# Performance work log

Measured on AMD Instinct MI355X. Metric: run time of the kernel, lower is better.

## Reference

```python
import jax, jax.numpy as jnp
import numpy as np

B, K, D = 8192, 8192, 512

def setup_inputs() -> dict:
    key = jax.random.key(0)
    k1, k2 = jax.random.split(key)
    z_e = jax.random.normal(k1, (B, D), dtype=jnp.float32)
    # codebook: kaiming-uniform-initialized parameter; random normal scaled similarly is fine for a numeric baseline
    codebook = jax.random.normal(k2, (K, D), dtype=jnp.float32)
    return {"z_e": z_e, "codebook": codebook}

def reference(z_e, codebook):
    # Euclidean distances via dot-product expansion (same math as
    # torch.norm(z_e[:,None]-codebook[None], dim=-1) without the [B,K,D] intermediate):
    # d^2 = ||z||^2 - 2 z.c + ||c||^2
    z_sq = jnp.sum(z_e * z_e, axis=-1, keepdims=True)          # [B,1]
    c_sq = jnp.sum(codebook * codebook, axis=-1)               # [K]
    cross = jnp.einsum('bd,kd->bk', z_e, codebook)             # [B,K] GEMM
    d2 = jnp.maximum(z_sq - 2.0 * cross + c_sq[None, :], 0.0)  # clamp fp negatives
    distances = jnp.sqrt(d2)                                   # [B,K]
    indices = jnp.argmin(distances, axis=-1)                   # [B]
    z_q = jnp.take(codebook, indices, axis=0)                  # [B,D] gather
    return (z_q, indices)
```

## Files before the change

### kernel.cpp

```cpp
#include <hip/hip_runtime.h>


constexpr int Bn = 8192;
constexpr int Kn = 8192;
constexpr int Dn = 512;

using half8  = __attribute__((ext_vector_type(8)))  _Float16;
using f32x16 = __attribute__((ext_vector_type(16))) float;

#define WS_CSQ  0u
#define WS_ZSQ  (32u*1024u)
#define WS_MAX  (64u*1024u)
#define WS_CNT  (64u*1024u + 64u)
#define WS_WL   (96u*1024u)
#define WS_PART (1u*1024u*1024u)
#define WS_P2   WS_PART
#define WS_CIMG (10u*1024u*1024u)
#define WS_ZIMG (18u*1024u*1024u)
#define WS_CEXT (26u*1024u*1024u)

typedef __attribute__((address_space(3))) void       as3_void;
typedef const __attribute__((address_space(1))) void as1_cvoid;

#define MFMA16 __builtin_amdgcn_mfma_f32_32x32x16_f16


__global__ __launch_bounds__(256) void prep_sums(const float* __restrict__ Z,
                                                 const float* __restrict__ Cb,
                                                 char* __restrict__ ws) {
  const int w = threadIdx.x >> 6, lane = threadIdx.x & 63;
  const int rid = blockIdx.x * 4 + w;
  if (blockIdx.x == 0 && threadIdx.x == 0) *(int*)(ws + WS_CNT) = 0;
  const bool isZ = rid < Bn;
  const int r = isZ ? rid : rid - Bn;
  const float* src = (isZ ? Z : Cb) + (size_t)r * Dn + lane * 8;
  const float4 v0 = *reinterpret_cast<const float4*>(src);
  const float4 v1 = *reinterpret_cast<const float4*>(src + 4);
  float ss = v0.x * v0.x + v0.y * v0.y + v0.z * v0.z + v0.w * v0.w +
             v1.x * v1.x + v1.y * v1.y + v1.z * v1.z + v1.w * v1.w;
#pragma unroll
  for (int off = 32; off; off >>= 1) ss += __shfl_xor(ss, off);
  if (lane == 0) {
    if (isZ) ((float*)(ws + WS_ZSQ))[r] = ss;
    else {
      ((float*)(ws + WS_CSQ))[r] = ss;
      atomicMax((int*)(ws + WS_MAX), __float_as_int(ss));
    }
  }
}

__global__ __launch_bounds__(256) void prep_img(const float* __restrict__ Z,
                                                const float* __restrict__ Cb,
                                                char* __restrict__ ws) {
  const int w = threadIdx.x >> 6, lane = threadIdx.x & 63;
  const int wid = blockIdx.x * 4 + w;
  char* CI = ws + WS_CIMG;
  char* ZI = ws + WS_ZIMG;
  char* CE = ws + WS_CEXT;
  if (wid < 2048) {
    const bool isC = wid < 1024;
    const int f = isC ? wid : wid - 1024;
    const int koct = f & 3;
    const int grp = isC ? ((f >> 2) & 3) : ((f >> 2) & 7);
    const int blk = isC ? (f >> 4) : (f >> 5);
    const int rowbase = (isC ? blk * 128 : blk * 256) + grp * 32;
    const float* src = isC ? Cb : Z;
    char* img = isC ? CI : ZI;
    const int fr = isC ? 256 : 512;
    const int ktsel = lane & 1, rr = lane >> 1;
    const float* rowp = src + (size_t)(rowbase + rr) * Dn;
#pragma unroll
    for (int kp = 0; kp < 4; ++kp) {
      const int kt = koct * 8 + kp * 2 + ktsel;
      const float4 v0 = *reinterpret_cast<const float4*>(rowp + kt * 16);
      const float4 v1 = *reinterpret_cast<const float4*>(rowp + kt * 16 + 4);
      const float4 v2 = *reinterpret_cast<const float4*>(rowp + kt * 16 + 8);
      const float4 v3 = *reinterpret_cast<const float4*>(rowp + kt * 16 + 12);
      const float fl[16] = {v0.x, v0.y, v0.z, v0.w, v1.x, v1.y, v1.z, v1.w,
                            v2.x, v2.y, v2.z, v2.w, v3.x, v3.y, v3.z, v3.w};
      _Float16 h[16];
#pragma unroll
      for (int j = 0; j < 16; ++j) h[j] = (_Float16)fl[j];
      const half8 lo8 = {h[0], h[1], h[2], h[3], h[4], h[5], h[6], h[7]};
      const half8 hi8 = {h[8], h[9], h[10], h[11], h[12], h[13], h[14], h[15]};
      char* fb = img + ((size_t)(blk * 32 + kt) * fr + grp * 64) * 16;
      *reinterpret_cast<half8*>(fb + rr * 16) = lo8;
      *reinterpret_cast<half8*>(fb + 512 + rr * 16) = hi8;
    }
  } else {
    const int e = wid - 2048;
    const int grp = e & 3, blk = e >> 2;
    half8 ev = {};
    if (lane < 32) {
      const float ss = ((const float*)(ws + WS_CSQ))[blk * 128 + grp * 32 + lane];
      const _Float16 hi = (_Float16)(-0.5f * ss);
      ev[0] = hi;
      ev[1] = (_Float16)(-0.5f * ss - (float)hi);
    }
    char* fb = CE + (size_t)(blk * 4 + grp) * 1024;
    *reinterpret_cast<half8*>(fb + lane * 16) = ev;
  }
}

__global__ __launch_bounds__(256, 2) void vq_pass1(char* __restrict__ ws) {
  __shared__ uint4 lds4[4096];
  char* lds = (char*)lds4;
  const int t = threadIdx.x, lane = t & 63, w = t >> 6;
  const int wm = w >> 1, wn = w & 1;
  const int bid = blockIdx.x;
  const int zblk = (bid & 7) * 4 + ((bid >> 3) & 3);
  const int split = bid >> 5;
  const int r31 = lane & 31, kh = lane >> 5;
  const size_t l16 = (size_t)lane * 16;

  const char* zsrcT = ws + WS_ZIMG + (size_t)zblk * 262144 + (size_t)w * 2048 + l16;
  char* const ldsW = lds + w * 2048;
  const char* APt = ws + WS_CIMG + (size_t)(split * 4) * 131072 + wm * 2048 + l16;
  const char* EbT = ws + WS_CEXT + (size_t)(split * 4) * 4096 + wm * 2048 + l16;
  const char* ldsRd = lds + wn * 4096 + kh * 512 + r31 * 16;

  half8 aset[4][2], aE[2];
  half8 bext = {};
  if (kh == 0) { bext[0] = (_Float16)1.f; bext[1] = (_Float16)1.f; }

  float qm1[4], qm2[4];
  int qi[4];
#pragma unroll
  for (int nb = 0; nb < 4; ++nb) { qm1[nb] = -3e38f; qm2[nb] = -3e38f; qi[nb] = 0x7fffffff; }
  f32x16 acc[2][4] = {};

#define GLDS(S, D) __builtin_amdgcn_global_load_lds((as1_cvoid*)(S), (as3_void*)(D), 16, 0, 0)

  GLDS(zsrcT, ldsW); GLDS(zsrcT + 1024, ldsW + 1024);
  aset[0][0] = *reinterpret_cast<const half8*>(APt);
  aset[0][1] = *reinterpret_cast<const half8*>(APt + 1024);
  GLDS(zsrcT + 8192, ldsW + 16384); GLDS(zsrcT + 8192 + 1024, ldsW + 16384 + 1024);
  aset[1][0] = *reinterpret_cast<const half8*>(APt + 4096);
  aset[1][1] = *reinterpret_cast<const half8*>(APt + 4096 + 1024);
  aE[0] = *reinterpret_cast<const half8*>(EbT);
  aE[1] = *reinterpret_cast<const half8*>(EbT + 1024);
  asm volatile("s_waitcnt vmcnt(8)" ::: "memory");
  __builtin_amdgcn_s_barrier();

  for (int p = 0; p < 4; ++p) {
#pragma unroll
    for (int kt = 0; kt < 32; ++kt) {
      {
        const char* An = (kt < 30) ? APt + (kt + 2) * 4096
                                   : APt + 131072 + (kt - 30) * 4096;
        aset[(kt + 2) & 3][0] = *reinterpret_cast<const half8*>(An);
        aset[(kt + 2) & 3][1] = *reinterpret_cast<const half8*>(An + 1024);
      }
      {
        const char* zs = zsrcT + ((kt + 2) & 31) * 8192;
        char* zd = ldsW + ((kt + 2) & 3) * 16384;
        GLDS(zs, zd); GLDS(zs + 1024, zd + 1024);
      }
      {
        const char* bb = ldsRd + (kt & 3) * 16384;
        const half8 b0 = *reinterpret_cast<const half8*>(bb);
        const half8 b1 = *reinterpret_cast<const half8*>(bb + 1024);
        const half8 b2 = *reinterpret_cast<const half8*>(bb + 2048);
        const half8 b3 = *reinterpret_cast<const half8*>(bb + 3072);
        const half8 a0 = aset[kt & 3][0];
        const half8 a1 = aset[kt & 3][1];
        acc[0][0] = MFMA16(a0, b0, acc[0][0], 0, 0, 0);
        acc[0][1] = MFMA16(a0, b1, acc[0][1], 0, 0, 0);
        acc[0][2] = MFMA16(a0, b2, acc[0][2], 0, 0, 0);
        acc[0][3] = MFMA16(a0, b3, acc[0][3], 0, 0, 0);
        acc[1][0] = MFMA16(a1, b0, acc[1][0], 0, 0, 0);
        acc[1][1] = MFMA16(a1, b1, acc[1][1], 0, 0, 0);
        acc[1][2] = MFMA16(a1, b2, acc[1][2], 0, 0, 0);
        acc[1][3] = MFMA16(a1, b3, acc[1][3], 0, 0, 0);
      }
      if (kt == 0) asm volatile("s_waitcnt vmcnt(6)" ::: "memory");
      else         asm volatile("s_waitcnt vmcnt(4)" ::: "memory");
      __builtin_amdgcn_s_barrier();
    }
#pragma unroll
    for (int nb = 0; nb < 4; ++nb) {
      acc[0][nb] = MFMA16(aE[0], bext, acc[0][nb], 0, 0, 0);
      acc[1][nb] = MFMA16(aE[1], bext, acc[1][nb], 0, 0, 0);
    }
    {
      const int cb = split * 512 + p * 128 + wm * 64 + 4 * kh;
#pragma unroll
      for (int nb = 0; nb < 4; ++nb) {
        float m1 = qm1[nb], m2 = qm2[nb];
        int i1 = qi[nb];
#pragma unroll
        for (int ms = 0; ms < 2; ++ms)
#pragma unroll
          for (int r = 0; r < 16; ++r) {
            const float a = acc[ms][nb][r];
            const int ci = cb + ms * 32 + (r & 3) + 8 * (r >> 2);
            const bool gt = (a > m1) || (a == m1 && ci < i1);
            const float nm2 = gt ? m1 : fmaxf(m2, a);
            m1 = gt ? a : m1;
            i1 = gt ? ci : i1;
            m2 = nm2;
          }
        qm1[nb] = m1; qm2[nb] = m2; qi[nb] = i1;
        acc[0][nb] = (f32x16)0.f;
        acc[1][nb] = (f32x16)0.f;
      }
    }
    APt += 131072;
    if (p < 3) {
      aE[0] = *reinterpret_cast<const half8*>(EbT + (p + 1) * 4096);
      aE[1] = *reinterpret_cast<const half8*>(EbT + (p + 1) * 4096 + 1024);
    }
  }
  asm volatile("s_waitcnt vmcnt(0)" ::: "memory");

  float4* part = (float4*)(ws + WS_PART);
  const int bucket = split * 4 + wm * 2 + kh;
#pragma unroll
  for (int nb = 0; nb < 4; ++nb) {
    const int row = zblk * 256 + wn * 128 + nb * 32 + r31;
    part[(size_t)row * 64 + bucket] =
        make_float4(-2.f * qm1[nb], (float)qi[nb], -2.f * qm2[nb], 0.f);
  }
#undef GLDS
}

__global__ __launch_bounds__(256) void gather_finalize(const float* __restrict__ Z,
                                                       const float* __restrict__ Cb,
                                                       char* __restrict__ ws,
                                                       float* __restrict__ zq,
                                                       float* __restrict__ idx_out) {
  const int w = threadIdx.x >> 6, l = threadIdx.x & 63;
  const int row = blockIdx.x * 4 + w;
  const float4 q = ((const float4*)(ws + WS_PART))[(size_t)row * 64 + l];
  float s1 = q.x;
  int i1 = (int)q.y;
#pragma unroll
  for (int off = 1; off <= 32; off <<= 1) {
    const float os = __shfl_xor(s1, off); const int oi = __shfl_xor(i1, off);
    if (os < s1 || (os == s1 && oi < i1)) { s1 = os; i1 = oi; }
  }
  const float zs = ((const float*)(ws + WS_ZSQ))[row];
  const float cmax = __int_as_float(*(const int*)(ws + WS_MAX));
  const float thr = s1 + 4.0e-3f * sqrtf(zs * cmax) + 0.05f;
  int cnt = (q.x <= thr ? 1 : 0) + (q.z <= thr ? 1 : 0);
  int hide = (q.z <= thr) ? 1 : 0;
#pragma unroll
  for (int off = 1; off <= 32; off <<= 1) {
    cnt += __shfl_xor(cnt, off);
    hide |= __shfl_xor(hide, off);
  }
  if (cnt >= 5 || hide) {
    if (l == 0) {
      const int pos = atomicAdd((int*)(ws + WS_CNT), 1);
      if (pos < Bn) ((int*)(ws + WS_WL))[pos] = row;
    }
    return;
  }
  const float* csq = (const float*)(ws + WS_CSQ);
  const float4 z0 = *reinterpret_cast<const float4*>(Z + (size_t)row * Dn + l * 8);
  const float4 z1 = *reinterpret_cast<const float4*>(Z + (size_t)row * Dn + l * 8 + 4);
  float mycand = (q.x <= thr) ? q.x : 3e38f;
  const int myid = (int)q.y;
  float best_s = 3e38f;
  int best_i = 0x7fffffff;
  for (int it = 0; it < 4; ++it) {
    float cs_ = mycand;
    int ci_ = myid;
#pragma unroll
    for (int off = 1; off <= 32; off <<= 1) {
      const float os = __shfl_xor(cs_, off); const int oi = __shfl_xor(ci_, off);
      if (os < cs_ || (os == cs_ && oi < ci_)) { cs_ = os; ci_ = oi; }
    }
    if (cs_ > thr) break;
    if (myid == ci_) mycand = 3e38f;
    const float4 c0 = *reinterpret_cast<const float4*>(Cb + (size_t)ci_ * Dn + l * 8);
    const float4 c1 = *reinterpret_cast<const float4*>(Cb + (size_t)ci_ * Dn + l * 8 + 4);
    float pa = z0.x * c0.x + z0.y * c0.y + z0.z * c0.z + z0.w * c0.w +
               z1.x * c1.x + z1.y * c1.y + z1.z * c1.z + z1.w * c1.w;
#pragma unroll
    for (int off = 1; off <= 32; off <<= 1) pa += __shfl_xor(pa, off);
    const float se = csq[ci_] - 2.f * pa;
    if (se < best_s || (se == best_s && ci_ < best_i)) { best_s = se; best_i = ci_; }
  }
  const float4 o0 = *reinterpret_cast<const float4*>(Cb + (size_t)best_i * Dn + l * 8);
  const float4 o1 = *reinterpret_cast<const float4*>(Cb + (size_t)best_i * Dn + l * 8 + 4);
  *reinterpret_cast<float4*>(zq + (size_t)row * Dn + l * 8) = o0;
  *reinterpret_cast<float4*>(zq + (size_t)row * Dn + l * 8 + 4) = o1;
  if (l == 0) idx_out[row] = (float)best_i;
}

__global__ __launch_bounds__(256) void rescue1(const float* __restrict__ Z,
                                               const float* __restrict__ Cb,
                                               char* __restrict__ ws) {
  const int cntRaw = *(const int*)(ws + WS_CNT);
  const int cnt = cntRaw > Bn ? Bn : cntRaw;
  if (cnt == 0) return;
  const int tiles_r = (cnt + 63) >> 6;
  const int total = tiles_r * 128;
  const int* wl = (const int*)(ws + WS_WL);
  const float* csq = (const float*)(ws + WS_CSQ);
  float2* p2 = (float2*)(ws + WS_P2);
  __shared__ float As[32][68];
  __shared__ float Bs[32][68];
  __shared__ int wlrows[64];
  const int t = threadIdx.x;
  const int tx = t & 15, ty = t >> 4;
  const int sr = t >> 3, sc = (t & 7) * 4;
  for (int tile = blockIdx.x; tile < total; tile += gridDim.x) {
    const int tr = tile >> 7, tc = tile & 127;
    __syncthreads();
    if (t < 64) {
      const int wi = tr * 64 + t;
      wlrows[t] = wl[wi < cnt ? wi : cnt - 1];
    }
    __syncthreads();
    float acc[4][4] = {};
    for (int k0 = 0; k0 < Dn; k0 += 32) {
#pragma unroll
      for (int rr = 0; rr < 2; ++rr) {
        const int m = sr + rr * 32;
        const float4 v = *reinterpret_cast<const float4*>(Z + (size_t)wlrows[m] * Dn + k0 + sc);
        As[sc + 0][m] = v.x; As[sc + 1][m] = v.y; As[sc + 2][m] = v.z; As[sc + 3][m] = v.w;
        const float4 u = *reinterpret_cast<const float4*>(Cb + (size_t)(tc * 64 + m) * Dn + k0 + sc);
        Bs[sc + 0][m] = u.x; Bs[sc + 1][m] = u.y; Bs[sc + 2][m] = u.z; Bs[sc + 3][m] = u.w;
      }
      __syncthreads();
#pragma unroll
      for (int k = 0; k < 32; ++k) {
        const float4 a = *reinterpret_cast<const float4*>(&As[k][ty * 4]);
        const float4 b = *reinterpret_cast<const float4*>(&Bs[k][tx * 4]);
        acc[0][0] += a.x * b.x; acc[0][1] += a.x * b.y; acc[0][2] += a.x * b.z; acc[0][3] += a.x * b.w;
        acc[1][0] += a.y * b.x; acc[1][1] += a.y * b.y; acc[1][2] += a.y * b.z; acc[1][3] += a.y * b.w;
        acc[2][0] += a.z * b.x; acc[2][1] += a.z * b.y; acc[2][2] += a.z * b.z; acc[2][3] += a.z * b.w;
        acc[3][0] += a.w * b.x; acc[3][1] += a.w * b.y; acc[3][2] += a.w * b.z; acc[3][3] += a.w * b.w;
      }
      __syncthreads();
    }
#pragma unroll
    for (int i = 0; i < 4; ++i) {
      float bsv = 3e38f;
      int bi = 0;
#pragma unroll
      for (int j = 0; j < 4; ++j) {
        const int n = tc * 64 + tx * 4 + j;
        const float s = csq[n] - 2.f * acc[i][j];
        if (s < bsv || (s == bsv && n < bi)) { bsv = s; bi = n; }
      }
#pragma unroll
      for (int off = 1; off <= 8; off <<= 1) {
        const float os = __shfl_xor(bsv, off); const int oi = __shfl_xor(bi, off);
        if (os < bsv || (os == bsv && oi < bi)) { bsv = os; bi = oi; }
      }
      if (tx == 0) p2[(size_t)(tr * 64 + ty * 4 + i) * 128 + tc] = make_float2(bsv, (float)bi);
    }
  }
}

__global__ __launch_bounds__(64) void rescue2(const float* __restrict__ Cb,
                                              char* __restrict__ ws,
                                              float* __restrict__ zq,
                                              float* __restrict__ idx_out) {
  const int cntRaw = *(const int*)(ws + WS_CNT);
  const int cnt = cntRaw > Bn ? Bn : cntRaw;
  const int* wl = (const int*)(ws + WS_WL);
  const float2* p2 = (const float2*)(ws + WS_P2);
  const int l = threadIdx.x;
  for (int rr = blockIdx.x; rr < cnt; rr += gridDim.x) {
    const int row = wl[rr];
    const float2 e1 = p2[(size_t)rr * 128 + l];
    const float2 e2 = p2[(size_t)rr * 128 + 64 + l];
    float bs_ = e1.x;
    int bi_ = (int)e1.y;
    if (e2.x < bs_ || (e2.x == bs_ && (int)e2.y < bi_)) { bs_ = e2.x; bi_ = (int)e2.y; }
#pragma unroll
    for (int off = 1; off <= 32; off <<= 1) {
      const float os = __shfl_xor(bs_, off); const int oi = __shfl_xor(bi_, off);
      if (os < bs_ || (os == bs_ && oi < bi_)) { bs_ = os; bi_ = oi; }
    }
    const float4 c0 = *reinterpret_cast<const float4*>(Cb + (size_t)bi_ * Dn + l * 8);
    const float4 c1 = *reinterpret_cast<const float4*>(Cb + (size_t)bi_ * Dn + l * 8 + 4);
    *reinterpret_cast<float4*>(zq + (size_t)row * Dn + l * 8) = c0;
    *reinterpret_cast<float4*>(zq + (size_t)row * Dn + l * 8 + 4) = c1;
    if (l == 0) idx_out[row] = (float)bi_;
  }
}

extern "C" void kernel_launch(void* const* d_in, const int* in_sizes, int n_in,
                              void* d_out, int out_size, void* d_ws, size_t ws_size,
                              hipStream_t stream) {
  const float* Z = (const float*)d_in[0];
  const float* C = (const float*)d_in[1];
  float* out = (float*)d_out;
  char* ws = (char*)d_ws;

  prep_sums<<<4096, 256, 0, stream>>>(Z, C, ws);
  prep_img<<<576, 256, 0, stream>>>(Z, C, ws);
  vq_pass1<<<512, 256, 0, stream>>>(ws);
  gather_finalize<<<2048, 256, 0, stream>>>(Z, C, ws, out, out + (size_t)Bn * Dn);
  rescue1<<<512, 256, 0, stream>>>(Z, C, ws);
  rescue2<<<256, 64, 0, stream>>>(C, ws, out, out + (size_t)Bn * Dn);
}
```

Baseline: 272.7 us.

## Track top-3 per bucket, halve LDS ring, and restructure pass1 pipeline

The main GEMM loop is flattened into 64 iterations that each process two k-tiles. The LDS ring shrinks to half size and there is one full vmcnt(0) wait plus barrier per iteration, with setprio raised around the MFMAs. The per-bucket running reduction now keeps the top-2 candidates with indices plus a third score. The finalize step can then verify up to two candidates per bucket and skip the exact recheck when only one candidate is within the threshold. This is meant to send fewer rows to the expensive fp32 rescue path and to skip redundant dot products. The costs are more register pressure, a stricter per-iteration memory wait that may expose load latency, and a widened threshold that may add verification work.

```diff
diff --git a/kernel.cpp b/kernel.cpp
--- a/kernel.cpp
+++ b/kernel.cpp
@@ -13,17 +13,17 @@
 #define WS_MAX  (64u*1024u)
 #define WS_CNT  (64u*1024u + 64u)
 #define WS_WL   (96u*1024u)
-#define WS_PART (1u*1024u*1024u)
-#define WS_P2   WS_PART
-#define WS_CIMG (10u*1024u*1024u)
-#define WS_ZIMG (18u*1024u*1024u)
-#define WS_CEXT (26u*1024u*1024u)
+#define WS_P1   (1u*1024u*1024u)
+#define WS_P3   (9u*1024u*1024u)
+#define WS_P2R  WS_P1
+#define WS_CIMG (13u*1024u*1024u)
+#define WS_ZIMG (21u*1024u*1024u)
+#define WS_CEXT (29u*1024u*1024u)
 
 typedef __attribute__((address_space(3))) void       as3_void;
 typedef const __attribute__((address_space(1))) void as1_cvoid;
 
 #define MFMA16 __builtin_amdgcn_mfma_f32_32x32x16_f16
-
 
 __global__ __launch_bounds__(256) void prep_sums(const float* __restrict__ Z,
                                                  const float* __restrict__ Cb,
@@ -103,7 +103,7 @@
 }
 
 __global__ __launch_bounds__(256, 2) void vq_pass1(char* __restrict__ ws) {
-  __shared__ uint4 lds4[4096];
+  __shared__ uint4 lds4[2048];
   char* lds = (char*)lds4;
   const int t = threadIdx.x, lane = t & 63, w = t >> 6;
   const int wm = w >> 1, wn = w & 1;
@@ -115,111 +115,121 @@
 
   const char* zsrcT = ws + WS_ZIMG + (size_t)zblk * 262144 + (size_t)w * 2048 + l16;
   char* const ldsW = lds + w * 2048;
-  const char* APt = ws + WS_CIMG + (size_t)(split * 4) * 131072 + wm * 2048 + l16;
-  const char* EbT = ws + WS_CEXT + (size_t)(split * 4) * 4096 + wm * 2048 + l16;
+  const char* APb = ws + WS_CIMG + (size_t)split * 524288 + wm * 2048 + l16;
+  const char* EbT = ws + WS_CEXT + (size_t)split * 16384 + wm * 2048 + l16;
   const char* ldsRd = lds + wn * 4096 + kh * 512 + r31 * 16;
 
   half8 aset[4][2], aE[2];
   half8 bext = {};
   if (kh == 0) { bext[0] = (_Float16)1.f; bext[1] = (_Float16)1.f; }
 
-  float qm1[4], qm2[4];
-  int qi[4];
-#pragma unroll
-  for (int nb = 0; nb < 4; ++nb) { qm1[nb] = -3e38f; qm2[nb] = -3e38f; qi[nb] = 0x7fffffff; }
+  float qm1[4], qm2[4], qm3[4];
+  int qi1[4], qi2[4];
+#pragma unroll
+  for (int nb = 0; nb < 4; ++nb) {
+    qm1[nb] = -3e38f; qm2[nb] = -3e38f; qm3[nb] = -3e38f;
+    qi1[nb] = 0x7fffffff; qi2[nb] = 0x7fffffff;
+  }
   f32x16 acc[2][4] = {};
 
 #define GLDS(S, D) __builtin_amdgcn_global_load_lds((as1_cvoid*)(S), (as3_void*)(D), 16, 0, 0)
 
   GLDS(zsrcT, ldsW); GLDS(zsrcT + 1024, ldsW + 1024);
-  aset[0][0] = *reinterpret_cast<const half8*>(APt);
-  aset[0][1] = *reinterpret_cast<const half8*>(APt + 1024);
-  GLDS(zsrcT + 8192, ldsW + 16384); GLDS(zsrcT + 8192 + 1024, ldsW + 16384 + 1024);
-  aset[1][0] = *reinterpret_cast<const half8*>(APt + 4096);
-  aset[1][1] = *reinterpret_cast<const half8*>(APt + 4096 + 1024);
+  GLDS(zsrcT + 8192, ldsW + 8192); GLDS(zsrcT + 8192 + 1024, ldsW + 8192 + 1024);
+  aset[0][0] = *reinterpret_cast<const half8*>(APb);
+  aset[0][1] = *reinterpret_cast<const half8*>(APb + 1024);
+  aset[1][0] = *reinterpret_cast<const half8*>(APb + 4096);
+  aset[1][1] = *reinterpret_cast<const half8*>(APb + 4096 + 1024);
   aE[0] = *reinterpret_cast<const half8*>(EbT);
   aE[1] = *reinterpret_cast<const half8*>(EbT + 1024);
-  asm volatile("s_waitcnt vmcnt(8)" ::: "memory");
+  asm volatile("s_waitcnt vmcnt(0)" ::: "memory");
   __builtin_amdgcn_s_barrier();
 
-  for (int p = 0; p < 4; ++p) {
-#pragma unroll
-    for (int kt = 0; kt < 32; ++kt) {
-      {
-        const char* An = (kt < 30) ? APt + (kt + 2) * 4096
-                                   : APt + 131072 + (kt - 30) * 4096;
-        aset[(kt + 2) & 3][0] = *reinterpret_cast<const half8*>(An);
-        aset[(kt + 2) & 3][1] = *reinterpret_cast<const half8*>(An + 1024);
-      }
-      {
-        const char* zs = zsrcT + ((kt + 2) & 31) * 8192;
-        char* zd = ldsW + ((kt + 2) & 3) * 16384;
+#pragma unroll 2
+  for (int iv = 0; iv < 64; ++iv) {
+    if (iv < 63) {
+#pragma unroll
+      for (int j = 0; j < 2; ++j) {
+        const int ft = 2 * iv + 2 + j;
+        const char* zs = zsrcT + (size_t)(ft & 31) * 8192;
+        char* zd = ldsW + (ft & 3) * 8192;
         GLDS(zs, zd); GLDS(zs + 1024, zd + 1024);
       }
-      {
-        const char* bb = ldsRd + (kt & 3) * 16384;
-        const half8 b0 = *reinterpret_cast<const half8*>(bb);
-        const half8 b1 = *reinterpret_cast<const half8*>(bb + 1024);
-        const half8 b2 = *reinterpret_cast<const half8*>(bb + 2048);
-        const half8 b3 = *reinterpret_cast<const half8*>(bb + 3072);
-        const half8 a0 = aset[kt & 3][0];
-        const half8 a1 = aset[kt & 3][1];
-        acc[0][0] = MFMA16(a0, b0, acc[0][0], 0, 0, 0);
-        acc[0][1] = MFMA16(a0, b1, acc[0][1], 0, 0, 0);
-        acc[0][2] = MFMA16(a0, b2, acc[0][2], 0, 0, 0);
-        acc[0][3] = MFMA16(a0, b3, acc[0][3], 0, 0, 0);
-        acc[1][0] = MFMA16(a1, b0, acc[1][0], 0, 0, 0);
-        acc[1][1] = MFMA16(a1, b1, acc[1][1], 0, 0, 0);
-        acc[1][2] = MFMA16(a1, b2, acc[1][2], 0, 0, 0);
-        acc[1][3] = MFMA16(a1, b3, acc[1][3], 0, 0, 0);
-      }
-      if (kt == 0) asm volatile("s_waitcnt vmcnt(6)" ::: "memory");
-      else         asm volatile("s_waitcnt vmcnt(4)" ::: "memory");
-      __builtin_amdgcn_s_barrier();
-    }
-#pragma unroll
-    for (int nb = 0; nb < 4; ++nb) {
-      acc[0][nb] = MFMA16(aE[0], bext, acc[0][nb], 0, 0, 0);
-      acc[1][nb] = MFMA16(aE[1], bext, acc[1][nb], 0, 0, 0);
-    }
-    {
+#pragma unroll
+      for (int j = 0; j < 2; ++j) {
+        const int ft = 2 * iv + 2 + j;
+        const char* s = APb + (size_t)ft * 4096;
+        aset[ft & 3][0] = *reinterpret_cast<const half8*>(s);
+        aset[ft & 3][1] = *reinterpret_cast<const half8*>(s + 1024);
+      }
+    }
+    __builtin_amdgcn_s_setprio(1);
+#pragma unroll
+    for (int j = 0; j < 2; ++j) {
+      const int ft = 2 * iv + j;
+      const char* bb = ldsRd + (ft & 3) * 8192;
+      const half8 b0 = *reinterpret_cast<const half8*>(bb);
+      const half8 b1 = *reinterpret_cast<const half8*>(bb + 1024);
+      const half8 b2 = *reinterpret_cast<const half8*>(bb + 2048);
+      const half8 b3 = *reinterpret_cast<const half8*>(bb + 3072);
+      const half8 a0 = aset[ft & 3][0];
+      const half8 a1 = aset[ft & 3][1];
+      acc[0][0] = MFMA16(a0, b0, acc[0][0], 0, 0, 0);
+      acc[0][1] = MFMA16(a0, b1, acc[0][1], 0, 0, 0);
+      acc[0][2] = MFMA16(a0, b2, acc[0][2], 0, 0, 0);
+      acc[0][3] = MFMA16(a0, b3, acc[0][3], 0, 0, 0);
+      acc[1][0] = MFMA16(a1, b0, acc[1][0], 0, 0, 0);
+      acc[1][1] = MFMA16(a1, b1, acc[1][1], 0, 0, 0);
+      acc[1][2] = MFMA16(a1, b2, acc[1][2], 0, 0, 0);
+      acc[1][3] = MFMA16(a1, b3, acc[1][3], 0, 0, 0);
+    }
+    __builtin_amdgcn_s_setprio(0);
+    if ((iv & 15) == 15) {
+      const int p = iv >> 4;
+#pragma unroll
+      for (int nb = 0; nb < 4; ++nb) {
+        acc[0][nb] = MFMA16(aE[0], bext, acc[0][nb], 0, 0, 0);
+        acc[1][nb] = MFMA16(aE[1], bext, acc[1][nb], 0, 0, 0);
+      }
       const int cb = split * 512 + p * 128 + wm * 64 + 4 * kh;
 #pragma unroll
       for (int nb = 0; nb < 4; ++nb) {
-        float m1 = qm1[nb], m2 = qm2[nb];
-        int i1 = qi[nb];
+        float m1 = qm1[nb], m2 = qm2[nb], m3 = qm3[nb];
+        int i1 = qi1[nb], i2 = qi2[nb];
 #pragma unroll
         for (int ms = 0; ms < 2; ++ms)
 #pragma unroll
           for (int r = 0; r < 16; ++r) {
             const float a = acc[ms][nb][r];
             const int ci = cb + ms * 32 + (r & 3) + 8 * (r >> 2);
-            const bool gt = (a > m1) || (a == m1 && ci < i1);
-            const float nm2 = gt ? m1 : fmaxf(m2, a);
-            m1 = gt ? a : m1;
-            i1 = gt ? ci : i1;
-            m2 = nm2;
+            const bool b1 = (a > m1) || (a == m1 && ci < i1);
+            const bool b2 = (a > m2) || (a == m2 && ci < i2);
+            m3 = b2 ? m2 : fmaxf(m3, a);
+            if (b1) { m2 = m1; i2 = i1; m1 = a; i1 = ci; }
+            else if (b2) { m2 = a; i2 = ci; }
           }
-        qm1[nb] = m1; qm2[nb] = m2; qi[nb] = i1;
+        qm1[nb] = m1; qm2[nb] = m2; qm3[nb] = m3; qi1[nb] = i1; qi2[nb] = i2;
         acc[0][nb] = (f32x16)0.f;
         acc[1][nb] = (f32x16)0.f;
       }
-    }
-    APt += 131072;
-    if (p < 3) {
-      aE[0] = *reinterpret_cast<const half8*>(EbT + (p + 1) * 4096);
-      aE[1] = *reinterpret_cast<const half8*>(EbT + (p + 1) * 4096 + 1024);
-    }
-  }
-  asm volatile("s_waitcnt vmcnt(0)" ::: "memory");
-
-  float4* part = (float4*)(ws + WS_PART);
+      if (p < 3) {
+        aE[0] = *reinterpret_cast<const half8*>(EbT + (p + 1) * 4096);
+        aE[1] = *reinterpret_cast<const half8*>(EbT + (p + 1) * 4096 + 1024);
+      }
+    }
+    asm volatile("s_waitcnt vmcnt(0)" ::: "memory");
+    __builtin_amdgcn_s_barrier();
+  }
+
+  float4* p1 = (float4*)(ws + WS_P1);
+  float2* p3 = (float2*)(ws + WS_P3);
   const int bucket = split * 4 + wm * 2 + kh;
 #pragma unroll
   for (int nb = 0; nb < 4; ++nb) {
     const int row = zblk * 256 + wn * 128 + nb * 32 + r31;
-    part[(size_t)row * 64 + bucket] =
-        make_float4(-2.f * qm1[nb], (float)qi[nb], -2.f * qm2[nb], 0.f);
+    p1[(size_t)row * 64 + bucket] =
+        make_float4(-2.f * qm1[nb], (float)qi1[nb], -2.f * qm2[nb], (float)qi2[nb]);
+    p3[(size_t)row * 64 + bucket] = make_float2(-2.f * qm3[nb], 0.f);
   }
 #undef GLDS
 }
@@ -231,7 +241,8 @@
                                                        float* __restrict__ idx_out) {
   const int w = threadIdx.x >> 6, l = threadIdx.x & 63;
   const int row = blockIdx.x * 4 + w;
-  const float4 q = ((const float4*)(ws + WS_PART))[(size_t)row * 64 + l];
+  const float4 q = ((const float4*)(ws + WS_P1))[(size_t)row * 64 + l];
+  const float s3 = ((const float2*)(ws + WS_P3))[(size_t)row * 64 + l].x;
   float s1 = q.x;
   int i1 = (int)q.y;
 #pragma unroll
@@ -241,52 +252,59 @@
   }
   const float zs = ((const float*)(ws + WS_ZSQ))[row];
   const float cmax = __int_as_float(*(const int*)(ws + WS_MAX));
-  const float thr = s1 + 4.0e-3f * sqrtf(zs * cmax) + 0.05f;
+  const float thr = s1 + 4.0e-3f * sqrtf(zs * cmax) + 0.10f;
   int cnt = (q.x <= thr ? 1 : 0) + (q.z <= thr ? 1 : 0);
-  int hide = (q.z <= thr) ? 1 : 0;
+  int hide = (s3 <= thr) ? 1 : 0;
 #pragma unroll
   for (int off = 1; off <= 32; off <<= 1) {
     cnt += __shfl_xor(cnt, off);
     hide |= __shfl_xor(hide, off);
   }
-  if (cnt >= 5 || hide) {
+  if (cnt > 6 || hide) {
     if (l == 0) {
       const int pos = atomicAdd((int*)(ws + WS_CNT), 1);
       if (pos < Bn) ((int*)(ws + WS_WL))[pos] = row;
     }
     return;
   }
-  const float* csq = (const float*)(ws + WS_CSQ);
-  const float4 z0 = *reinterpret_cast<const float4*>(Z + (size_t)row * Dn + l * 8);
-  const float4 z1 = *reinterpret_cast<const float4*>(Z + (size_t)row * Dn + l * 8 + 4);
-  float mycand = (q.x <= thr) ? q.x : 3e38f;
-  const int myid = (int)q.y;
-  float best_s = 3e38f;
-  int best_i = 0x7fffffff;
-  for (int it = 0; it < 4; ++it) {
-    float cs_ = mycand;
-    int ci_ = myid;
-#pragma unroll
-    for (int off = 1; off <= 32; off <<= 1) {
-      const float os = __shfl_xor(cs_, off); const int oi = __shfl_xor(ci_, off);
-      if (os < cs_ || (os == cs_ && oi < ci_)) { cs_ = os; ci_ = oi; }
-    }
-    if (cs_ > thr) break;
-    if (myid == ci_) mycand = 3e38f;
-    const float4 c0 = *reinterpret_cast<const float4*>(Cb + (size_t)ci_ * Dn + l * 8);
-    const float4 c1 = *reinterpret_cast<const float4*>(Cb + (size_t)ci_ * Dn + l * 8 + 4);
-    float pa = z0.x * c0.x + z0.y * c0.y + z0.z * c0.z + z0.w * c0.w +
-               z1.x * c1.x + z1.y * c1.y + z1.z * c1.z + z1.w * c1.w;
-#pragma unroll
-    for (int off = 1; off <= 32; off <<= 1) pa += __shfl_xor(pa, off);
-    const float se = csq[ci_] - 2.f * pa;
-    if (se < best_s || (se == best_s && ci_ < best_i)) { best_s = se; best_i = ci_; }
-  }
-  const float4 o0 = *reinterpret_cast<const float4*>(Cb + (size_t)best_i * Dn + l * 8);
-  const float4 o1 = *reinterpret_cast<const float4*>(Cb + (size_t)best_i * Dn + l * 8 + 4);
+  int winner = i1;
+  if (cnt > 1) {
+    const float* csq = (const float*)(ws + WS_CSQ);
+    const float4 z0 = *reinterpret_cast<const float4*>(Z + (size_t)row * Dn + l * 8);
+    const float4 z1 = *reinterpret_cast<const float4*>(Z + (size_t)row * Dn + l * 8 + 4);
+    float pa_s = (q.x <= thr) ? q.x : 3e38f;
+    float pb_s = (q.z <= thr) ? q.z : 3e38f;
+    const int pa_i = (int)q.y, pb_i = (int)q.w;
+    float best_s = 3e38f;
+    int best_i = 0x7fffffff;
+    for (int it = 0; it < 6; ++it) {
+      float cs_; int ci_;
+      if (pb_s < pa_s || (pb_s == pa_s && pb_i < pa_i)) { cs_ = pb_s; ci_ = pb_i; }
+      else { cs_ = pa_s; ci_ = pa_i; }
+#pragma unroll
+      for (int off = 1; off <= 32; off <<= 1) {
+        const float os = __shfl_xor(cs_, off); const int oi = __shfl_xor(ci_, off);
+        if (os < cs_ || (os == cs_ && oi < ci_)) { cs_ = os; ci_ = oi; }
+      }
+      if (cs_ > thr) break;
+      if (ci_ == pa_i) pa_s = 3e38f;
+      if (ci_ == pb_i) pb_s = 3e38f;
+      const float4 c0 = *reinterpret_cast<const float4*>(Cb + (size_t)ci_ * Dn + l * 8);
+      const float4 c1 = *reinterpret_cast<const float4*>(Cb + (size_t)ci_ * Dn + l * 8 + 4);
+      float pa = z0.x * c0.x + z0.y * c0.y + z0.z * c0.z + z0.w * c0.w +
+                 z1.x * c1.x + z1.y * c1.y + z1.z * c1.z + z1.w * c1.w;
+#pragma unroll
+      for (int off = 1; off <= 32; off <<= 1) pa += __shfl_xor(pa, off);
+      const float se = csq[ci_] - 2.f * pa;
+      if (se < best_s || (se == best_s && ci_ < best_i)) { best_s = se; best_i = ci_; }
+    }
+    winner = best_i;
+  }
+  const float4 o0 = *reinterpret_cast<const float4*>(Cb + (size_t)winner * Dn + l * 8);
+  const float4 o1 = *reinterpret_cast<const float4*>(Cb + (size_t)winner * Dn + l * 8 + 4);
   *reinterpret_cast<float4*>(zq + (size_t)row * Dn + l * 8) = o0;
   *reinterpret_cast<float4*>(zq + (size_t)row * Dn + l * 8 + 4) = o1;
-  if (l == 0) idx_out[row] = (float)best_i;
+  if (l == 0) idx_out[row] = (float)winner;
 }
 
 __global__ __launch_bounds__(256) void rescue1(const float* __restrict__ Z,
@@ -299,7 +317,7 @@
   const int total = tiles_r * 128;
   const int* wl = (const int*)(ws + WS_WL);
   const float* csq = (const float*)(ws + WS_CSQ);
-  float2* p2 = (float2*)(ws + WS_P2);
+  float2* p2 = (float2*)(ws + WS_P2R);
   __shared__ float As[32][68];
   __shared__ float Bs[32][68];
   __shared__ int wlrows[64];
@@ -363,7 +381,7 @@
   const int cntRaw = *(const int*)(ws + WS_CNT);
   const int cnt = cntRaw > Bn ? Bn : cntRaw;
   const int* wl = (const int*)(ws + WS_WL);
-  const float2* p2 = (const float2*)(ws + WS_P2);
+  const float2* p2 = (const float2*)(ws + WS_P2R);
   const int l = threadIdx.x;
   for (int rr = blockIdx.x; rr < cnt; rr += gridDim.x) {
     const int row = wl[rr];
```

After: 361.9 us. 1.33x slower.
